# Optimization experiments

Hardware: AMD Instinct MI355X
Metric: run time of the kernel (lower is better)

## Reference

```python
import jax, jax.numpy as jnp
import numpy as np

KY = KX = 7
PAD_Y = (KY - 1) // 2
PAD_X = (KX - 1) // 2
SIGMA_COLOR = 0.1
SIGMA_SPACE = (1.5, 1.5)


def _gaussian1d(ksize, sigma):
    x = jnp.arange(ksize, dtype=jnp.float32) - float(ksize // 2)
    g = jnp.exp(-jnp.square(x) / (2.0 * sigma * sigma))
    return g / jnp.sum(g)


def setup_inputs() -> dict:
    key = jax.random.key(0)
    x = jax.random.uniform(key, (8, 3, 512, 512), dtype=jnp.float32)
    return {"input": x}


def reference(input) -> jnp.ndarray:
    B, C, H, W = input.shape
    padded = jnp.pad(input, ((0, 0), (0, 0), (PAD_Y, PAD_Y), (PAD_X, PAD_X)), mode="reflect")
    # patches[b,c,h,w,k] = padded[b,c,h+i,w+j], k = i*KX + j  (ky-major, matches torch unfold)
    patches = jnp.stack(
        [padded[:, :, i:i + H, j:j + W] for i in range(KY) for j in range(KX)],
        axis=-1,
    )  # (B, C, H, W, KY*KX)
    diff = patches - input[..., None]
    # l1 color distance, squared: (sum_c |diff|)^2 -> (B,1,H,W,K)
    color_dist_sq = jnp.square(jnp.sum(jnp.abs(diff), axis=1, keepdims=True))
    color_kernel = jnp.exp((-0.5 / (SIGMA_COLOR ** 2)) * color_dist_sq)
    ky1d = _gaussian1d(KY, SIGMA_SPACE[0])
    kx1d = _gaussian1d(KX, SIGMA_SPACE[1])
    space_kernel = (ky1d[:, None] * kx1d[None, :]).reshape(1, 1, 1, 1, KY * KX)
    kernel = space_kernel * color_kernel  # (B,1,H,W,K)
    out = jnp.sum(patches * kernel, axis=-1) / jnp.sum(kernel, axis=-1)
    return out
```

## Files before the change

### kernel.cpp

```cpp
#include <hip/hip_runtime.h>

#define HH 512
#define WW 512
#define CH 3
#define BX 64
#define BY 4
#define TX (BX + 6)
#define TY (BY + 6)
#define NELEM (CH * TY * TX)

__global__ __launch_bounds__(BX * BY)
void bilateral_kernel(const float* __restrict__ in, float* __restrict__ out) {
    __shared__ float sm[CH][TY][TX];

    const int bx0 = blockIdx.x * BX;
    const int by0 = blockIdx.y * BY;
    const int b   = blockIdx.z;
    const int tid = threadIdx.y * BX + threadIdx.x;

    const float* inb = in + (size_t)b * CH * HH * WW;

    float* smf = &sm[0][0][0];
    for (int idx = tid; idx < NELEM; idx += BX * BY) {
        int c  = idx / (TY * TX);
        int r  = idx - c * (TY * TX);
        int ty = r / TX;
        int tx = r - ty * TX;
        int gy = by0 + ty - 3;
        int gx = bx0 + tx - 3;
        gy = (gy < 0) ? -gy : ((gy >= HH) ? 2 * (HH - 1) - gy : gy);
        gx = (gx < 0) ? -gx : ((gx >= WW) ? 2 * (WW - 1) - gx : gx);
        smf[idx] = inb[(c * HH + gy) * WW + gx];
    }
    __syncthreads();

    const int lx = threadIdx.x;
    const int ly = threadIdx.y;

    const float c0 = sm[0][ly + 3][lx + 3];
    const float c1 = sm[1][ly + 3][lx + 3];
    const float c2 = sm[2][ly + 3][lx + 3];

    float n0 = 0.f, n1 = 0.f, n2 = 0.f, den = 0.f;

#pragma unroll
    for (int i = 0; i < 7; ++i) {
#pragma unroll
        for (int j = 0; j < 7; ++j) {
            const float p0 = sm[0][ly + i][lx + j];
            const float p1 = sm[1][ly + i][lx + j];
            const float p2 = sm[2][ly + i][lx + j];
            const float d  = fabsf(p0 - c0) + fabsf(p1 - c1) + fabsf(p2 - c2);
            const float lnw = -(float)((i - 3) * (i - 3) + (j - 3) * (j - 3)) * (1.0f / 4.5f);
            const float w = __expf(fmaf(d * d, -50.0f, lnw));
            n0 = fmaf(w, p0, n0);
            n1 = fmaf(w, p1, n1);
            n2 = fmaf(w, p2, n2);
            den += w;
        }
    }

    const float inv = 1.0f / den;
    const int y = by0 + ly;
    const int x = bx0 + lx;
    float* outb = out + (size_t)b * CH * HH * WW;
    outb[(0 * HH + y) * WW + x] = n0 * inv;
    outb[(1 * HH + y) * WW + x] = n1 * inv;
    outb[(2 * HH + y) * WW + x] = n2 * inv;
}

extern "C" void kernel_launch(void* const* d_in, const int* in_sizes, int n_in,
                              void* d_out, int out_size, void* d_ws, size_t ws_size,
                              hipStream_t stream) {
    const float* in = (const float*)d_in[0];
    float* out = (float*)d_out;
    const int B = in_sizes[0] / (CH * HH * WW);
    dim3 grid(WW / BX, HH / BY, B);
    dim3 block(BX, BY, 1);
    bilateral_kernel<<<grid, block, 0, stream>>>(in, out);
}
```

Baseline: 52.38 us.

## Compute four pixels per thread with register row reuse and float4 smem loads

```diff
diff --git a/kernel.cpp b/kernel.cpp
--- a/kernel.cpp
+++ b/kernel.cpp
@@ -3,70 +3,115 @@
 #define HH 512
 #define WW 512
 #define CH 3
-#define BX 64
-#define BY 4
-#define TX (BX + 6)
-#define TY (BY + 6)
-#define NELEM (CH * TY * TX)
+#define NTX 64
+#define NTY 4
+#define PX  4
+#define TILE_W  (NTX * PX + 6)
+#define TILE_WP 264
+#define TILE_H  (NTY + 6)
 
-__global__ __launch_bounds__(BX * BY)
+#define K1 (-72.13475204444817f)
+#define K2 (-0.3205988979753252f)
+
+__device__ __forceinline__ int reflect_idx(int v, int n) {
+    v = (v < 0) ? -v : v;
+    return (v >= n) ? (2 * (n - 1) - v) : v;
+}
+
+__device__ __forceinline__ float fast_exp2(float x) {
+#if __has_builtin(__builtin_amdgcn_exp2f)
+    return __builtin_amdgcn_exp2f(x);
+#else
+    return exp2f(x);
+#endif
+}
+
+__global__ __launch_bounds__(NTX * NTY)
 void bilateral_kernel(const float* __restrict__ in, float* __restrict__ out) {
-    __shared__ float sm[CH][TY][TX];
+    __shared__ __align__(16) float sm[CH][TILE_H][TILE_WP];
 
-    const int bx0 = blockIdx.x * BX;
-    const int by0 = blockIdx.y * BY;
+    const int bx0 = blockIdx.x * (NTX * PX);
+    const int by0 = blockIdx.y * NTY;
     const int b   = blockIdx.z;
-    const int tid = threadIdx.y * BX + threadIdx.x;
-
     const float* inb = in + (size_t)b * CH * HH * WW;
 
-    float* smf = &sm[0][0][0];
-    for (int idx = tid; idx < NELEM; idx += BX * BY) {
-        int c  = idx / (TY * TX);
-        int r  = idx - c * (TY * TX);
-        int ty = r / TX;
-        int tx = r - ty * TX;
-        int gy = by0 + ty - 3;
-        int gx = bx0 + tx - 3;
-        gy = (gy < 0) ? -gy : ((gy >= HH) ? 2 * (HH - 1) - gy : gy);
-        gx = (gx < 0) ? -gx : ((gx >= WW) ? 2 * (WW - 1) - gx : gx);
-        smf[idx] = inb[(c * HH + gy) * WW + gx];
+    for (int c = 0; c < CH; ++c) {
+        for (int ty = threadIdx.y; ty < TILE_H; ty += NTY) {
+            const int gy = reflect_idx(by0 + ty - 3, HH);
+            const float* grow = inb + (c * HH + gy) * WW;
+            float* srow = &sm[c][ty][0];
+            for (int tx = threadIdx.x; tx < TILE_WP; tx += NTX) {
+                const int gx = reflect_idx(bx0 + tx - 3, WW);
+                srow[tx] = grow[gx];
+            }
+        }
     }
     __syncthreads();
 
     const int lx = threadIdx.x;
     const int ly = threadIdx.y;
+    const int cb = PX * lx;
 
-    const float c0 = sm[0][ly + 3][lx + 3];
-    const float c1 = sm[1][ly + 3][lx + 3];
-    const float c2 = sm[2][ly + 3][lx + 3];
+    float c0[PX], c1[PX], c2[PX];
+#pragma unroll
+    for (int p = 0; p < PX; ++p) {
+        c0[p] = sm[0][ly + 3][cb + 3 + p];
+        c1[p] = sm[1][ly + 3][cb + 3 + p];
+        c2[p] = sm[2][ly + 3][cb + 3 + p];
+    }
 
-    float n0 = 0.f, n1 = 0.f, n2 = 0.f, den = 0.f;
+    float n0[PX] = {0,0,0,0}, n1[PX] = {0,0,0,0}, n2[PX] = {0,0,0,0}, den[PX] = {0,0,0,0};
 
 #pragma unroll
     for (int i = 0; i < 7; ++i) {
+        float A0[12], A1[12], A2[12];
+#define LOADROW(DST, CHI)                                                        \
+        {                                                                        \
+            const float4 q0 = *reinterpret_cast<const float4*>(&sm[CHI][ly + i][cb]);      \
+            const float4 q1 = *reinterpret_cast<const float4*>(&sm[CHI][ly + i][cb + 4]);  \
+            const float4 q2 = *reinterpret_cast<const float4*>(&sm[CHI][ly + i][cb + 8]);  \
+            DST[0] = q0.x; DST[1] = q0.y; DST[2]  = q0.z; DST[3]  = q0.w;        \
+            DST[4] = q1.x; DST[5] = q1.y; DST[6]  = q1.z; DST[7]  = q1.w;        \
+            DST[8] = q2.x; DST[9] = q2.y; DST[10] = q2.z; DST[11] = q2.w;        \
+        }
+        LOADROW(A0, 0)
+        LOADROW(A1, 1)
+        LOADROW(A2, 2)
+#undef LOADROW
+
 #pragma unroll
-        for (int j = 0; j < 7; ++j) {
-            const float p0 = sm[0][ly + i][lx + j];
-            const float p1 = sm[1][ly + i][lx + j];
-            const float p2 = sm[2][ly + i][lx + j];
-            const float d  = fabsf(p0 - c0) + fabsf(p1 - c1) + fabsf(p2 - c2);
-            const float lnw = -(float)((i - 3) * (i - 3) + (j - 3) * (j - 3)) * (1.0f / 4.5f);
-            const float w = __expf(fmaf(d * d, -50.0f, lnw));
-            n0 = fmaf(w, p0, n0);
-            n1 = fmaf(w, p1, n1);
-            n2 = fmaf(w, p2, n2);
-            den += w;
+        for (int p = 0; p < PX; ++p) {
+#pragma unroll
+            for (int j = 0; j < 7; ++j) {
+                const float v0 = A0[p + j];
+                const float v1 = A1[p + j];
+                const float v2 = A2[p + j];
+                const float d  = fabsf(v0 - c0[p]) + fabsf(v1 - c1[p]) + fabsf(v2 - c2[p]);
+                const float r2 = (float)((i - 3) * (i - 3) + (j - 3) * (j - 3));
+                const float w  = fast_exp2(fmaf(d * d, K1, r2 * K2));
+                n0[p]  = fmaf(w, v0, n0[p]);
+                n1[p]  = fmaf(w, v1, n1[p]);
+                n2[p]  = fmaf(w, v2, n2[p]);
+                den[p] += w;
+            }
         }
     }
 
-    const float inv = 1.0f / den;
-    const int y = by0 + ly;
-    const int x = bx0 + lx;
+    const int y  = by0 + ly;
+    const int x0 = bx0 + PX * lx;
     float* outb = out + (size_t)b * CH * HH * WW;
-    outb[(0 * HH + y) * WW + x] = n0 * inv;
-    outb[(1 * HH + y) * WW + x] = n1 * inv;
-    outb[(2 * HH + y) * WW + x] = n2 * inv;
+
+    float inv[PX];
+#pragma unroll
+    for (int p = 0; p < PX; ++p) inv[p] = 1.0f / den[p];
+
+    float4 o;
+    o.x = n0[0] * inv[0]; o.y = n0[1] * inv[1]; o.z = n0[2] * inv[2]; o.w = n0[3] * inv[3];
+    *reinterpret_cast<float4*>(&outb[(0 * HH + y) * WW + x0]) = o;
+    o.x = n1[0] * inv[0]; o.y = n1[1] * inv[1]; o.z = n1[2] * inv[2]; o.w = n1[3] * inv[3];
+    *reinterpret_cast<float4*>(&outb[(1 * HH + y) * WW + x0]) = o;
+    o.x = n2[0] * inv[0]; o.y = n2[1] * inv[1]; o.z = n2[2] * inv[2]; o.w = n2[3] * inv[3];
+    *reinterpret_cast<float4*>(&outb[(2 * HH + y) * WW + x0]) = o;
 }
 
 extern "C" void kernel_launch(void* const* d_in, const int* in_sizes, int n_in,
@@ -75,7 +120,7 @@
     const float* in = (const float*)d_in[0];
     float* out = (float*)d_out;
     const int B = in_sizes[0] / (CH * HH * WW);
-    dim3 grid(WW / BX, HH / BY, B);
-    dim3 block(BX, BY, 1);
+    dim3 grid(WW / (NTX * PX), HH / NTY, B);
+    dim3 block(NTX, NTY, 1);
     bilateral_kernel<<<grid, block, 0, stream>>>(in, out);
 }
```

Measured after the change: 96.41 us. 1.84x slower.
